# Optimization experiments

Hardware: AMD Instinct MI355X
Metric: run time of the kernel (lower is better)

The kernel has to match this reference:

```python
import jax, jax.numpy as jnp
import numpy as np

B, N, D, DG = 32, 2048, 512, 1024


def layernorm(x, g, b, eps=1e-5):
    m = jnp.mean(x, axis=-1, keepdims=True)
    v = jnp.mean((x - m) ** 2, axis=-1, keepdims=True)
    return (x - m) * jax.lax.rsqrt(v + eps) * g + b


def simple_rms_norm(x, eps=1e-6):
    # parameter-free RMSNorm used inside Hgru1d
    return x * jax.lax.rsqrt(jnp.mean(x * x, axis=-1, keepdims=True) + eps)


def linear_recurrence(lam, u, reverse):
    # h_t = lam_t * h_{t-1} + u_t along axis=1, via associative scan
    def comb(c1, c2):
        a1, b1 = c1
        a2, b2 = c2
        return a1 * a2, a2 * b1 + b2
    return jax.lax.associative_scan(comb, (lam, u), axis=1, reverse=reverse)[1]


def hgru1d(x, lower_bound, Wi, bi, Wf, bf, Wg, bg, Wo, bo):
    # HGRN-style gated recurrence, bidirectional (causal=False, shared params)
    i = jax.nn.silu(x @ Wi + bi)                       # candidate input  [b,n,d]
    f = jax.nn.sigmoid(x @ Wf + bf)                    # forget gate      [b,n,d]
    lam = lower_bound + (1.0 - lower_bound) * f        # lower-bounded decay
    u = (1.0 - lam) * i
    h = linear_recurrence(lam, u, False) + linear_recurrence(lam, u, True)
    h = simple_rms_norm(h)
    g = jax.nn.sigmoid(x @ Wg + bg)                    # output gate
    return (h * g) @ Wo + bo


def glu(x, W1, b1, W2, b2, W3, b3):
    return (jax.nn.silu(x @ W1 + b1) * (x @ W2 + b2)) @ W3 + b3


def setup_inputs() -> dict:
    key = jax.random.key(0)
    ks = jax.random.split(key, 16)
    s = 0.02
    return {
        "x": jax.random.normal(ks[0], (B, N, D), dtype=jnp.float32),
        "lower_bound": 0,
        "Wi": jax.random.normal(ks[1], (D, D), jnp.float32) * s,
        "bi": jnp.zeros((D,), jnp.float32),
        "Wf": jax.random.normal(ks[2], (D, D), jnp.float32) * s,
        "bf": jnp.zeros((D,), jnp.float32),
        "Wg": jax.random.normal(ks[3], (D, D), jnp.float32) * s,
        "bg": jnp.zeros((D,), jnp.float32),
        "Wo": jax.random.normal(ks[4], (D, D), jnp.float32) * s,
        "bo": jnp.zeros((D,), jnp.float32),
        "tn_g": jnp.ones((D,), jnp.float32),
        "tn_b": jnp.zeros((D,), jnp.float32),
        "fn_g": jnp.ones((D,), jnp.float32),
        "fn_b": jnp.zeros((D,), jnp.float32),
        "W1": jax.random.normal(ks[5], (D, DG), jnp.float32) * s,
        "b1": jnp.zeros((DG,), jnp.float32),
        "W2": jax.random.normal(ks[6], (D, DG), jnp.float32) * s,
        "b2": jnp.zeros((DG,), jnp.float32),
        "W3": jax.random.normal(ks[7], (DG, D), jnp.float32) * s,
        "b3": jnp.zeros((D,), jnp.float32),
    }


def reference(x, lower_bound, Wi, bi, Wf, bf, Wg, bg, Wo, bo,
              tn_g, tn_b, fn_g, fn_b, W1, b1, W2, b2, W3, b3):
    lb = jnp.float32(lower_bound)
    # post-norm residual block
    x = x + layernorm(hgru1d(x, lb, Wi, bi, Wf, bf, Wg, bg, Wo, bo), tn_g, tn_b)
    x = x + layernorm(glu(x, W1, b1, W2, b2, W3, b3), fn_g, fn_b)
    return x
```

## Files before the change

kernel.cpp:

```cpp
#include <hip/hip_runtime.h>
#include <hip/hip_bf16.h>

#define BB 32
#define NN 2048
#define DD 512
#define DGG 1024
#define CC 32
#define LLEN 64

typedef short bf16x8 __attribute__((ext_vector_type(8)));
typedef float f32x4  __attribute__((ext_vector_type(4)));

__device__ __forceinline__ unsigned short f2bf(float f){
    __hip_bfloat16 h = __float2bfloat16(f);
    return *reinterpret_cast<unsigned short*>(&h);
}
__device__ __forceinline__ float bf2f(unsigned short u){
    unsigned int x = ((unsigned int)u) << 16;
    return __uint_as_float(x);
}
__device__ __forceinline__ float sigm(float x){ return 1.0f/(1.0f + __expf(-x)); }

__device__ __forceinline__ void gl_lds16(const unsigned short* g, unsigned short* l){
    __builtin_amdgcn_global_load_lds(
        (const __attribute__((address_space(1))) unsigned int*)g,
        (__attribute__((address_space(3))) unsigned int*)l, 16, 0, 0);
}

__global__ __launch_bounds__(256)
void wt_prep(const float* __restrict__ in, unsigned short* __restrict__ out,
             int K, int N)
{
    __shared__ float t[32][33];
    const int tid = threadIdx.x;
    const int r = tid >> 3;
    const int c = (tid & 7) << 2;
    const int n0 = blockIdx.x * 32;
    const int k0 = blockIdx.y * 32;
    float4 v = *(const float4*)(in + (size_t)(k0 + r) * N + n0 + c);
    t[r][c] = v.x; t[r][c+1] = v.y; t[r][c+2] = v.z; t[r][c+3] = v.w;
    __syncthreads();
    ushort4 o;
    o.x = f2bf(t[c+0][r]); o.y = f2bf(t[c+1][r]);
    o.z = f2bf(t[c+2][r]); o.w = f2bf(t[c+3][r]);
    *(ushort4*)(out + (size_t)(n0 + r) * K + k0 + c) = o;
}

__global__ __launch_bounds__(256)
void cast_bf16(const float* __restrict__ in, unsigned short* __restrict__ out)
{
    size_t i = ((size_t)blockIdx.x * 256 + threadIdx.x) * 4;
    float4 v = *(const float4*)(in + i);
    ushort4 o;
    o.x = f2bf(v.x); o.y = f2bf(v.y); o.z = f2bf(v.z); o.w = f2bf(v.w);
    *(ushort4*)(out + i) = o;
}

template<int MODE>
__global__ __launch_bounds__(256)
void gemm128(const unsigned short* __restrict__ A,
             const unsigned short* __restrict__ Bt,
             const float* __restrict__ bias,
             const unsigned short* __restrict__ staged,
             unsigned short* __restrict__ out0,
             unsigned short* __restrict__ out1,
             const int* __restrict__ lbp, int K, int Nn)
{
    __shared__ unsigned short As[128 * 32];
    __shared__ unsigned short Bs[128 * 32];

    const int tid  = threadIdx.x;
    const int wave = tid >> 6;
    const int lane = tid & 63;
    const int m0   = blockIdx.y * 128;
    const int n0   = blockIdx.x * 128;
    const int wr   = (wave >> 1) * 64;
    const int wc   = (wave & 1) * 64;
    const int lm   = lane & 15;
    const int quad = lane >> 4;

    f32x4 acc[4][4];
    const f32x4 zero = {0.f, 0.f, 0.f, 0.f};
    #pragma unroll
    for (int i = 0; i < 4; ++i)
        for (int j = 0; j < 4; ++j) acc[i][j] = zero;

    const int srow = wave * 32 + (lane >> 2);
    const int skof = (lane & 3) << 3;
    const unsigned short* ga0 = A  + (size_t)(m0 + srow) * K + skof;
    const unsigned short* ga1 = ga0 + (size_t)16 * K;
    const unsigned short* gb0 = Bt + (size_t)(n0 + srow) * K + skof;
    const unsigned short* gb1 = gb0 + (size_t)16 * K;
    unsigned short* la0 = &As[(wave * 32) * 32];
    unsigned short* la1 = &As[(wave * 32 + 16) * 32];
    unsigned short* lb0 = &Bs[(wave * 32) * 32];
    unsigned short* lb1 = &Bs[(wave * 32 + 16) * 32];

    for (int k0 = 0; k0 < K; k0 += 32) {
        gl_lds16(ga0, la0); gl_lds16(ga1, la1);
        gl_lds16(gb0, lb0); gl_lds16(gb1, lb1);
        ga0 += 32; ga1 += 32; gb0 += 32; gb1 += 32;
        __syncthreads();

        bf16x8 a[4], b[4];
        #pragma unroll
        for (int mi = 0; mi < 4; ++mi)
            a[mi] = *(const bf16x8*)&As[(wr + mi * 16 + lm) * 32 + quad * 8];
        #pragma unroll
        for (int ni = 0; ni < 4; ++ni)
            b[ni] = *(const bf16x8*)&Bs[(wc + ni * 16 + lm) * 32 + quad * 8];
        #pragma unroll
        for (int mi = 0; mi < 4; ++mi)
            #pragma unroll
            for (int ni = 0; ni < 4; ++ni)
                acc[mi][ni] = __builtin_amdgcn_mfma_f32_16x16x32_bf16(a[mi], b[ni], acc[mi][ni], 0, 0, 0);
        __syncthreads();
    }

    float lbv = 0.f;
    if constexpr (MODE == 3) lbv = (float)(*lbp);

    #pragma unroll
    for (int mi = 0; mi < 4; ++mi) {
        #pragma unroll
        for (int ni = 0; ni < 4; ++ni) {
            int col = n0 + wc + ni * 16 + lm;
            float bcol = bias[col];
            #pragma unroll
            for (int r = 0; r < 4; ++r) {
                int row = m0 + wr + mi * 16 + quad * 4 + r;
                size_t oidx = (size_t)row * Nn + col;
                float v = acc[mi][ni][r] + bcol;
                if constexpr (MODE == 0) {
                    out0[oidx] = f2bf(v);
                } else if constexpr (MODE == 1) {
                    out0[oidx] = f2bf(v * sigm(v));
                } else if constexpr (MODE == 2) {
                    out0[oidx] = f2bf(sigm(v));
                } else if constexpr (MODE == 3) {
                    float fv = sigm(v);
                    float lamv = lbv + (1.f - lbv) * fv;
                    float si = bf2f(staged[oidx]);
                    out0[oidx] = f2bf(lamv);
                    out1[oidx] = f2bf((1.f - lamv) * si);
                } else {
                    out0[oidx] = f2bf(bf2f(staged[oidx]) * v);
                }
            }
        }
    }
}

__global__ __launch_bounds__(512)
void scan_agg(const unsigned short* __restrict__ lam, const unsigned short* __restrict__ u,
              float* __restrict__ Aarr, float* __restrict__ Vf, float* __restrict__ Vr)
{
    int bc = blockIdx.x;
    int b = bc >> 5, c = bc & 31;
    int d = threadIdx.x;
    size_t base = ((size_t)b * NN + c * LLEN) * DD + d;
    float A = 1.f, vf = 0.f, vr = 0.f;
    for (int t = 0; t < LLEN; ++t) {
        float lv = bf2f(lam[base + (size_t)t * DD]);
        float uv = bf2f(u[base + (size_t)t * DD]);
        vf = lv * vf + uv;
        vr += uv * A;
        A *= lv;
    }
    size_t o = (size_t)bc * DD + d;
    Aarr[o] = A; Vf[o] = vf; Vr[o] = vr;
}

__global__ __launch_bounds__(256)
void scan_comb(const float* __restrict__ Aarr, const float* __restrict__ Vf,
               const float* __restrict__ Vr, float* __restrict__ cf, float* __restrict__ cr)
{
    int g = blockIdx.x * 256 + threadIdx.x;
    int b = g >> 9, d = g & 511;
    float S = 0.f;
    for (int c = 0; c < CC; ++c) {
        size_t o = (size_t)(b * CC + c) * DD + d;
        cf[o] = S;
        S = Vf[o] + Aarr[o] * S;
    }
    S = 0.f;
    for (int c = CC - 1; c >= 0; --c) {
        size_t o = (size_t)(b * CC + c) * DD + d;
        cr[o] = S;
        S = Vr[o] + Aarr[o] * S;
    }
}

__global__ __launch_bounds__(256)
void scan_final(const unsigned short* __restrict__ lam, const unsigned short* __restrict__ u,
                const float* __restrict__ cf, const float* __restrict__ cr,
                float* __restrict__ h)
{
    int bid = blockIdx.x;
    int dh = bid & 1, c = (bid >> 1) & 31, b = bid >> 6;
    int d = dh * 256 + threadIdx.x;
    size_t base = ((size_t)b * NN + c * LLEN) * DD + d;
    size_t co   = (size_t)(b * CC + c) * DD + d;

    float hbuf[LLEN];
    float hf = cf[co];
    #pragma unroll
    for (int t = 0; t < LLEN; ++t) {
        float lv = bf2f(lam[base + (size_t)t * DD]);
        float uv = bf2f(u[base + (size_t)t * DD]);
        hf = lv * hf + uv;
        hbuf[t] = hf;
    }
    float hr = cr[co];
    #pragma unroll
    for (int t = LLEN - 1; t >= 0; --t) {
        float lv = bf2f(lam[base + (size_t)t * DD]);
        float uv = bf2f(u[base + (size_t)t * DD]);
        hr = lv * hr + uv;
        h[base + (size_t)t * DD] = hbuf[t] + hr;
    }
}

__global__ __launch_bounds__(256)
void rms_mul(const float* __restrict__ h, const unsigned short* __restrict__ g,
             unsigned short* __restrict__ hg)
{
    int row = blockIdx.x;
    size_t base = (size_t)row * DD;
    int tid = threadIdx.x, col = tid * 2;
    float2 v = *(const float2*)&h[base + col];
    float ss = v.x * v.x + v.y * v.y;
    #pragma unroll
    for (int off = 32; off > 0; off >>= 1) ss += __shfl_down(ss, off);
    __shared__ float ps[4];
    __shared__ float scale_s;
    if ((tid & 63) == 0) ps[tid >> 6] = ss;
    __syncthreads();
    if (tid == 0) scale_s = rsqrtf((ps[0] + ps[1] + ps[2] + ps[3]) * (1.f / DD) + 1e-6f);
    __syncthreads();
    float sc = scale_s;
    ushort2 gv = *(const ushort2*)&g[base + col];
    ushort2 o;
    o.x = f2bf(v.x * sc * bf2f(gv.x));
    o.y = f2bf(v.y * sc * bf2f(gv.y));
    *(ushort2*)&hg[base + col] = o;
}

__global__ __launch_bounds__(256)
void add_ln(const float* __restrict__ xin, const unsigned short* __restrict__ y,
            const float* __restrict__ gam, const float* __restrict__ bet,
            float* __restrict__ out, unsigned short* __restrict__ outb)
{
    int row = blockIdx.x;
    size_t base = (size_t)row * DD;
    int tid = threadIdx.x, col = tid * 2;
    ushort2 yv = *(const ushort2*)&y[base + col];
    float vx = bf2f(yv.x), vy = bf2f(yv.y);
    float s = vx + vy;
    float ss = vx * vx + vy * vy;
    #pragma unroll
    for (int off = 32; off > 0; off >>= 1) {
        s  += __shfl_down(s, off);
        ss += __shfl_down(ss, off);
    }
    __shared__ float ps[8];
    __shared__ float stats[2];
    if ((tid & 63) == 0) { ps[tid >> 6] = s; ps[4 + (tid >> 6)] = ss; }
    __syncthreads();
    if (tid == 0) {
        float st  = ps[0] + ps[1] + ps[2] + ps[3];
        float sst = ps[4] + ps[5] + ps[6] + ps[7];
        float mean = st * (1.f / DD);
        float var  = sst * (1.f / DD) - mean * mean;
        stats[0] = mean; stats[1] = rsqrtf(var + 1e-5f);
    }
    __syncthreads();
    float mean = stats[0], inv = stats[1];
    float2 xv = *(const float2*)&xin[base + col];
    float2 gv = *(const float2*)&gam[col];
    float2 bv = *(const float2*)&bet[col];
    float2 o;
    o.x = xv.x + (vx - mean) * inv * gv.x + bv.x;
    o.y = xv.y + (vy - mean) * inv * gv.y + bv.y;
    *(float2*)&out[base + col] = o;
    if (outb) {
        ushort2 ob; ob.x = f2bf(o.x); ob.y = f2bf(o.y);
        *(ushort2*)&outb[base + col] = ob;
    }
}

extern "C" void kernel_launch(void* const* d_in, const int* in_sizes, int n_in,
                              void* d_out, int out_size, void* d_ws, size_t ws_size,
                              hipStream_t stream)
{
    const float* x   = (const float*)d_in[0];
    const int*   lb  = (const int*)d_in[1];
    const float* Wi  = (const float*)d_in[2];
    const float* bi  = (const float*)d_in[3];
    const float* Wf  = (const float*)d_in[4];
    const float* bfp = (const float*)d_in[5];
    const float* Wg  = (const float*)d_in[6];
    const float* bg  = (const float*)d_in[7];
    const float* Wo  = (const float*)d_in[8];
    const float* bo  = (const float*)d_in[9];
    const float* tng = (const float*)d_in[10];
    const float* tnb = (const float*)d_in[11];
    const float* fng = (const float*)d_in[12];
    const float* fnb = (const float*)d_in[13];
    const float* W1  = (const float*)d_in[14];
    const float* b1  = (const float*)d_in[15];
    const float* W2  = (const float*)d_in[16];
    const float* b2  = (const float*)d_in[17];
    const float* W3  = (const float*)d_in[18];
    const float* b3  = (const float*)d_in[19];

    unsigned short* wbase = (unsigned short*)d_ws;
    unsigned short* WiT = wbase;
    unsigned short* WfT = WiT + 262144;
    unsigned short* WgT = WfT + 262144;
    unsigned short* WoT = WgT + 262144;
    unsigned short* W1T = WoT + 262144;
    unsigned short* W2T = W1T + 524288;
    unsigned short* W3T = W2T + 524288;
    const size_t WTOT = 4 * 262144 + 3 * 524288;

    wt_prep<<<dim3(16, 16), 256, 0, stream>>>(Wi, WiT, 512, 512);
    wt_prep<<<dim3(16, 16), 256, 0, stream>>>(Wf, WfT, 512, 512);
    wt_prep<<<dim3(16, 16), 256, 0, stream>>>(Wg, WgT, 512, 512);
    wt_prep<<<dim3(16, 16), 256, 0, stream>>>(Wo, WoT, 512, 512);
    wt_prep<<<dim3(32, 16), 256, 0, stream>>>(W1, W1T, 512, 1024);
    wt_prep<<<dim3(32, 16), 256, 0, stream>>>(W2, W2T, 512, 1024);
    wt_prep<<<dim3(16, 32), 256, 0, stream>>>(W3, W3T, 1024, 512);

    const size_t perB = (size_t)4 * NN * DD * 2 + (size_t)5 * CC * DD * 4;
    int Bch = 32;
    while (Bch > 1 && WTOT * 2 + (size_t)Bch * perB > ws_size) Bch >>= 1;
    const int nch = BB / Bch;

    const size_t slabE = (size_t)Bch * NN * DD;

    for (int ch = 0; ch < nch; ++ch) {
        const size_t r0 = (size_t)ch * Bch * NN;
        const int Mc = Bch * NN;
        const float* xc = x + r0 * DD;
        unsigned short* S0 = wbase + WTOT;
        unsigned short* S1 = S0 + slabE;
        unsigned short* S2 = S0 + 2 * slabE;
        unsigned short* S3 = S0 + 3 * slabE;
        float* small = (float*)(S0 + 4 * slabE);
        const size_t agg = (size_t)Bch * CC * DD;
        float* Aarr = small;
        float* VfP  = small + agg;
        float* VrP  = small + 2 * agg;
        float* cfP  = small + 3 * agg;
        float* crP  = small + 4 * agg;
        float* hout = (float*)d_out + r0 * DD;

        cast_bf16<<<Mc / 2, 256, 0, stream>>>(xc, S3);
        gemm128<1><<<dim3(DD / 128, Mc / 128), 256, 0, stream>>>(
            S3, WiT, bi, nullptr, S0, nullptr, nullptr, DD, DD);
        gemm128<3><<<dim3(DD / 128, Mc / 128), 256, 0, stream>>>(
            S3, WfT, bfp, S0, S1, S0, lb, DD, DD);
        gemm128<2><<<dim3(DD / 128, Mc / 128), 256, 0, stream>>>(
            S3, WgT, bg, nullptr, S2, nullptr, nullptr, DD, DD);
        scan_agg<<<Bch * CC, 512, 0, stream>>>(S1, S0, Aarr, VfP, VrP);
        scan_comb<<<(Bch * DD) / 256, 256, 0, stream>>>(Aarr, VfP, VrP, cfP, crP);
        scan_final<<<Bch * CC * 2, 256, 0, stream>>>(S1, S0, cfP, crP, hout);
        rms_mul<<<Mc, 256, 0, stream>>>(hout, S2, S2);
        gemm128<0><<<dim3(DD / 128, Mc / 128), 256, 0, stream>>>(
            S2, WoT, bo, nullptr, S0, nullptr, nullptr, DD, DD);
        add_ln<<<Mc, 256, 0, stream>>>(xc, S0, tng, tnb, hout, S3);
        gemm128<1><<<dim3(DGG / 128, Mc / 128), 256, 0, stream>>>(
            S3, W1T, b1, nullptr, S1, nullptr, nullptr, DD, DGG);
        gemm128<4><<<dim3(DGG / 128, Mc / 128), 256, 0, stream>>>(
            S3, W2T, b2, S1, S1, nullptr, nullptr, DD, DGG);
        gemm128<0><<<dim3(DD / 128, Mc / 128), 256, 0, stream>>>(
            S1, W3T, b3, nullptr, S0, nullptr, nullptr, DGG, DD);
        add_ln<<<Mc, 256, 0, stream>>>(hout, S0, fng, fnb, hout, nullptr);
    }
}
```

Baseline: 1.293 ms.

## Replace 128x128 GEMM with 256x256 triple-buffered swizzled-LDS GEMM kernel

Replaces the 128x128-tile, 256-thread GEMM with a 256x256-tile, 512-thread kernel whose K and N are template parameters. It triple-buffers LDS with async global-to-LDS loads and a vmcnt-based wait, so each barrier is shared with prefetching two stages ahead. It also XOR-swizzles the LDS column slots to cut bank conflicts and remaps workgroups with an 8-way interleave for better cache locality. Larger tiles raise operand reuse but use more registers (128 accumulator floats) and 96KB of LDS per block, which may limit occupancy.

```diff
diff --git a/kernel.cpp b/kernel.cpp
--- a/kernel.cpp
+++ b/kernel.cpp
@@ -56,81 +56,114 @@
     *(ushort4*)(out + i) = o;
 }
 
-template<int MODE>
-__global__ __launch_bounds__(256)
-void gemm128(const unsigned short* __restrict__ A,
+template<int MODE, int K, int Nn>
+__global__ __launch_bounds__(512, 2)
+void gemm256(const unsigned short* __restrict__ A,
              const unsigned short* __restrict__ Bt,
              const float* __restrict__ bias,
              const unsigned short* __restrict__ staged,
              unsigned short* __restrict__ out0,
              unsigned short* __restrict__ out1,
-             const int* __restrict__ lbp, int K, int Nn)
-{
-    __shared__ unsigned short As[128 * 32];
-    __shared__ unsigned short Bs[128 * 32];
+             const int* __restrict__ lbp, int Mtiles)
+{
+    constexpr int NT   = K / 32;
+    constexpr int Ntl  = Nn / 256;
+    constexpr int TILE = 256 * 32;
+    __shared__ unsigned short AsE[3 * TILE];
+    __shared__ unsigned short BsE[3 * TILE];
 
     const int tid  = threadIdx.x;
     const int wave = tid >> 6;
     const int lane = tid & 63;
-    const int m0   = blockIdx.y * 128;
-    const int n0   = blockIdx.x * 128;
-    const int wr   = (wave >> 1) * 64;
-    const int wc   = (wave & 1) * 64;
     const int lm   = lane & 15;
     const int quad = lane >> 4;
-
-    f32x4 acc[4][4];
+    const int wr   = (wave >> 2) * 128;
+    const int wc   = (wave & 3) * 64;
+
+    const int nwg = Mtiles * Ntl;
+    const int h   = blockIdx.x;
+    const int wg  = (h & 7) * (nwg >> 3) + (h >> 3);
+    const int bm  = wg / Ntl;
+    const int bn  = wg - bm * Ntl;
+    const size_t m0 = (size_t)bm * 256;
+    const int    n0 = bn * 256;
+
+    const int lrow  = lane >> 2;
+    const int oslot = ((lane & 3) ^ ((lane >> 3) & 3)) << 3;
+    const unsigned short* gA = A  + (m0 + (size_t)(wave * 16 + lrow)) * K + oslot;
+    const unsigned short* gB = Bt + ((size_t)n0 + wave * 16 + lrow) * K + oslot;
+    unsigned short* lA = &AsE[(wave * 16) * 32];
+    unsigned short* lB = &BsE[(wave * 16) * 32];
+    const int aslot = (quad ^ ((lm >> 1) & 3)) << 3;
+
+    f32x4 acc[8][4];
     const f32x4 zero = {0.f, 0.f, 0.f, 0.f};
     #pragma unroll
-    for (int i = 0; i < 4; ++i)
+    for (int i = 0; i < 8; ++i)
+        #pragma unroll
         for (int j = 0; j < 4; ++j) acc[i][j] = zero;
 
-    const int srow = wave * 32 + (lane >> 2);
-    const int skof = (lane & 3) << 3;
-    const unsigned short* ga0 = A  + (size_t)(m0 + srow) * K + skof;
-    const unsigned short* ga1 = ga0 + (size_t)16 * K;
-    const unsigned short* gb0 = Bt + (size_t)(n0 + srow) * K + skof;
-    const unsigned short* gb1 = gb0 + (size_t)16 * K;
-    unsigned short* la0 = &As[(wave * 32) * 32];
-    unsigned short* la1 = &As[(wave * 32 + 16) * 32];
-    unsigned short* lb0 = &Bs[(wave * 32) * 32];
-    unsigned short* lb1 = &Bs[(wave * 32 + 16) * 32];
-
-    for (int k0 = 0; k0 < K; k0 += 32) {
-        gl_lds16(ga0, la0); gl_lds16(ga1, la1);
-        gl_lds16(gb0, lb0); gl_lds16(gb1, lb1);
-        ga0 += 32; ga1 += 32; gb0 += 32; gb1 += 32;
-        __syncthreads();
-
-        bf16x8 a[4], b[4];
+    #define STAGE(kt, bs) do {                                   \
+        const unsigned short* ga_ = gA + (kt) * 32;              \
+        const unsigned short* gb_ = gB + (kt) * 32;              \
+        unsigned short* la_ = lA + (bs) * TILE;                  \
+        unsigned short* lb_ = lB + (bs) * TILE;                  \
+        gl_lds16(ga_,           la_);                            \
+        gl_lds16(ga_ + 128 * K, la_ + 128 * 32);                 \
+        gl_lds16(gb_,           lb_);                            \
+        gl_lds16(gb_ + 128 * K, lb_ + 128 * 32);                 \
+    } while (0)
+
+    STAGE(0, 0);
+    STAGE(1, 1);
+    asm volatile("s_waitcnt vmcnt(4)" ::: "memory");
+    __builtin_amdgcn_s_barrier();
+
+    int br = 0;
+    for (int t = 0; t < NT; ++t) {
+        int bs = br + 2; if (bs >= 3) bs -= 3;
+        if (t + 2 < NT) STAGE(t + 2, bs);
+
+        const unsigned short* Ab = &AsE[br * TILE];
+        const unsigned short* Bb = &BsE[br * TILE];
+        bf16x8 a[8], b[4];
         #pragma unroll
-        for (int mi = 0; mi < 4; ++mi)
-            a[mi] = *(const bf16x8*)&As[(wr + mi * 16 + lm) * 32 + quad * 8];
+        for (int mi = 0; mi < 8; ++mi)
+            a[mi] = *(const bf16x8*)&Ab[(wr + mi * 16 + lm) * 32 + aslot];
         #pragma unroll
         for (int ni = 0; ni < 4; ++ni)
-            b[ni] = *(const bf16x8*)&Bs[(wc + ni * 16 + lm) * 32 + quad * 8];
+            b[ni] = *(const bf16x8*)&Bb[(wc + ni * 16 + lm) * 32 + aslot];
         #pragma unroll
-        for (int mi = 0; mi < 4; ++mi)
+        for (int mi = 0; mi < 8; ++mi)
             #pragma unroll
             for (int ni = 0; ni < 4; ++ni)
-                acc[mi][ni] = __builtin_amdgcn_mfma_f32_16x16x32_bf16(a[mi], b[ni], acc[mi][ni], 0, 0, 0);
-        __syncthreads();
-    }
+                acc[mi][ni] = __builtin_amdgcn_mfma_f32_16x16x32_bf16(
+                    a[mi], b[ni], acc[mi][ni], 0, 0, 0);
+
+        if (t + 2 < NT)      asm volatile("s_waitcnt vmcnt(4)" ::: "memory");
+        else if (t + 1 < NT) asm volatile("s_waitcnt vmcnt(0)" ::: "memory");
+        if (t + 1 < NT) __builtin_amdgcn_s_barrier();
+        br += 1; if (br == 3) br = 0;
+    }
+    #undef STAGE
 
     float lbv = 0.f;
     if constexpr (MODE == 3) lbv = (float)(*lbp);
 
-    #pragma unroll
-    for (int mi = 0; mi < 4; ++mi) {
+    float bcol[4];
+    #pragma unroll
+    for (int ni = 0; ni < 4; ++ni) bcol[ni] = bias[n0 + wc + ni * 16 + lm];
+
+    #pragma unroll
+    for (int mi = 0; mi < 8; ++mi) {
         #pragma unroll
         for (int ni = 0; ni < 4; ++ni) {
-            int col = n0 + wc + ni * 16 + lm;
-            float bcol = bias[col];
+            const int col = n0 + wc + ni * 16 + lm;
             #pragma unroll
             for (int r = 0; r < 4; ++r) {
-                int row = m0 + wr + mi * 16 + quad * 4 + r;
-                size_t oidx = (size_t)row * Nn + col;
-                float v = acc[mi][ni][r] + bcol;
+                const size_t row = m0 + wr + mi * 16 + quad * 4 + r;
+                const size_t oidx = row * Nn + col;
+                float v = acc[mi][ni][r] + bcol[ni];
                 if constexpr (MODE == 0) {
                     out0[oidx] = f2bf(v);
                 } else if constexpr (MODE == 1) {
@@ -342,6 +375,7 @@
     for (int ch = 0; ch < nch; ++ch) {
         const size_t r0 = (size_t)ch * Bch * NN;
         const int Mc = Bch * NN;
+        const int Mt = Mc / 256;
         const float* xc = x + r0 * DD;
         unsigned short* S0 = wbase + WTOT;
         unsigned short* S1 = S0 + slabE;
@@ -357,25 +391,25 @@
         float* hout = (float*)d_out + r0 * DD;
 
         cast_bf16<<<Mc / 2, 256, 0, stream>>>(xc, S3);
-        gemm128<1><<<dim3(DD / 128, Mc / 128), 256, 0, stream>>>(
-            S3, WiT, bi, nullptr, S0, nullptr, nullptr, DD, DD);
-        gemm128<3><<<dim3(DD / 128, Mc / 128), 256, 0, stream>>>(
-            S3, WfT, bfp, S0, S1, S0, lb, DD, DD);
-        gemm128<2><<<dim3(DD / 128, Mc / 128), 256, 0, stream>>>(
-            S3, WgT, bg, nullptr, S2, nullptr, nullptr, DD, DD);
+        gemm256<1, 512, 512><<<Mt * 2, 512, 0, stream>>>(
+            S3, WiT, bi, nullptr, S0, nullptr, nullptr, Mt);
+        gemm256<3, 512, 512><<<Mt * 2, 512, 0, stream>>>(
+            S3, WfT, bfp, S0, S1, S0, lb, Mt);
+        gemm256<2, 512, 512><<<Mt * 2, 512, 0, stream>>>(
+            S3, WgT, bg, nullptr, S2, nullptr, nullptr, Mt);
         scan_agg<<<Bch * CC, 512, 0, stream>>>(S1, S0, Aarr, VfP, VrP);
         scan_comb<<<(Bch * DD) / 256, 256, 0, stream>>>(Aarr, VfP, VrP, cfP, crP);
         scan_final<<<Bch * CC * 2, 256, 0, stream>>>(S1, S0, cfP, crP, hout);
         rms_mul<<<Mc, 256, 0, stream>>>(hout, S2, S2);
-        gemm128<0><<<dim3(DD / 128, Mc / 128), 256, 0, stream>>>(
-            S2, WoT, bo, nullptr, S0, nullptr, nullptr, DD, DD);
+        gemm256<0, 512, 512><<<Mt * 2, 512, 0, stream>>>(
+            S2, WoT, bo, nullptr, S0, nullptr, nullptr, Mt);
         add_ln<<<Mc, 256, 0, stream>>>(xc, S0, tng, tnb, hout, S3);
-        gemm128<1><<<dim3(DGG / 128, Mc / 128), 256, 0, stream>>>(
-            S3, W1T, b1, nullptr, S1, nullptr, nullptr, DD, DGG);
-        gemm128<4><<<dim3(DGG / 128, Mc / 128), 256, 0, stream>>>(
-            S3, W2T, b2, S1, S1, nullptr, nullptr, DD, DGG);
-        gemm128<0><<<dim3(DD / 128, Mc / 128), 256, 0, stream>>>(
-            S1, W3T, b3, nullptr, S0, nullptr, nullptr, DGG, DD);
+        gemm256<1, 512, 1024><<<Mt * 4, 512, 0, stream>>>(
+            S3, W1T, b1, nullptr, S1, nullptr, nullptr, Mt);
+        gemm256<4, 512, 1024><<<Mt * 4, 512, 0, stream>>>(
+            S3, W2T, b2, S1, S1, nullptr, nullptr, Mt);
+        gemm256<0, 1024, 512><<<Mt * 2, 512, 0, stream>>>(
+            S1, W3T, b3, nullptr, S0, nullptr, nullptr, Mt);
         add_ln<<<Mc, 256, 0, stream>>>(hout, S0, fng, fnb, hout, nullptr);
     }
 }
```

Measured after the change: 1.202 ms. 1.08x faster.
